# Kernel tuning notes

Hardware: AMD Instinct MI355X
Metric: run time of the kernel (lower is better)

The kernel has to match this reference:

```python
import jax, jax.numpy as jnp
import numpy as np

N_FFT = 1024
HOP = 256
WIN_LENGTH = 1024
B = 16
T = 480000


def setup_inputs() -> dict:
    key = jax.random.key(0)
    k1, k2 = jax.random.split(key)
    x = jax.random.normal(k1, (B, T), dtype=jnp.float32)
    window = jax.random.uniform(k2, (WIN_LENGTH,), dtype=jnp.float32)
    return {"x": x, "window": window}


def _dft_kernels(window):
    # pad window to n_fft if needed (here win_length == n_fft)
    if WIN_LENGTH < N_FFT:
        pl = (N_FFT - WIN_LENGTH) // 2
        window = jnp.pad(window, (pl, N_FFT - WIN_LENGTH - pl))
    n_freq = N_FFT // 2 + 1
    k = jnp.arange(n_freq, dtype=jnp.float32)[:, None]   # [F,1]
    n = jnp.arange(N_FFT, dtype=jnp.float32)[None, :]    # [1,N]
    basis = (2.0 * np.pi / N_FFT) * k * n                # [F,N]
    cos_k = jnp.cos(basis) * window[None, :]
    sin_k = -jnp.sin(basis) * window[None, :]
    return cos_k, sin_k


def reference(x, window):
    pad = N_FFT // 2
    xp = jnp.pad(x, ((0, 0), (pad, pad)), mode="reflect")  # center=True, reflect
    n_frames = (xp.shape[1] - N_FFT) // HOP + 1
    # frame extraction: [n_frames, n_fft] gather indices (strided windows)
    idx = jnp.arange(n_frames)[:, None] * HOP + jnp.arange(N_FFT)[None, :]
    frames = xp[:, idx]                                   # [B, n_frames, n_fft]
    cos_k, sin_k = _dft_kernels(window)                   # [F, n_fft]
    real = jnp.einsum("btn,fn->btf", frames, cos_k)        # [B, n_frames, F]
    imag = jnp.einsum("btn,fn->btf", frames, sin_k)
    return jnp.stack([real, imag], axis=-1)               # [B, n_frames, F, 2]
```

## Files before the change

kernel.cpp:

```cpp
#include <hip/hip_runtime.h>

#define BATCH     16
#define T_LEN     480000
#define PAD       512
#define TPAD      481024
#define HOP       256
#define NFRAMES   1876
#define NOUTROW   1026
#define KTOT      1024
#define NCOLS     1152

#define BM        256
#define BN        128
#define BK        32
#define KSTEPS    (KTOT / BK)
#define MTILES    8
#define ACHUNKS   8288
#define ABYTES    (ACHUNKS * 16)
#define BBUF      8192
#define NBUF      3
#define LDSBYTES  (ABYTES + NBUF * BBUF)
#define XPSTRIDE  493568

typedef __attribute__((ext_vector_type(8))) short short8;
typedef __attribute__((ext_vector_type(4))) float floatx4;

__device__ __forceinline__ unsigned short f2bf(float f) {
  union { float f; unsigned int u; } v; v.f = f;
  unsigned int u = v.u;
  return (unsigned short)((u + 0x7FFFu + ((u >> 16) & 1u)) >> 16);
}

__global__ __launch_bounds__(256) void build_xp(const float* __restrict__ x,
                                                unsigned short* __restrict__ xp) {
  const int i0 = (blockIdx.x * 256 + threadIdx.x) * 8;
  const int b  = blockIdx.y;
  const float* xb = x + (size_t)b * T_LEN;
  const int j0 = i0 - PAD;
  union { short8 v; unsigned short u[8]; } o;
  if (j0 >= 0 && j0 + 8 <= T_LEN) {
    const float4 lo = *(const float4*)(xb + j0);
    const float4 hi = *(const float4*)(xb + j0 + 4);
    o.u[0] = f2bf(lo.x); o.u[1] = f2bf(lo.y); o.u[2] = f2bf(lo.z); o.u[3] = f2bf(lo.w);
    o.u[4] = f2bf(hi.x); o.u[5] = f2bf(hi.y); o.u[6] = f2bf(hi.z); o.u[7] = f2bf(hi.w);
  } else {
#pragma unroll
    for (int e = 0; e < 8; ++e) {
      const int i = i0 + e;
      unsigned short v = 0;
      if (i < TPAD) {
        int j = i - PAD;
        if (j < 0) j = -j;
        if (j >= T_LEN) j = 2 * T_LEN - 2 - j;
        v = f2bf(xb[j]);
      }
      o.u[e] = v;
    }
  }
  *(short8*)(xp + (size_t)b * XPSTRIDE + i0) = o.v;
}

__global__ __launch_bounds__(256) void build_bmat(const float* __restrict__ win,
                                                  unsigned short* __restrict__ bm) {
  const int id = blockIdx.x * 256 + threadIdx.x;
  const int j  = id >> 7;
  const int k0 = (id & 127) * 8;
  union { short8 v; unsigned short u[8]; } o;
  if (j < NOUTROW) {
    const int f = j >> 1;
    const float4 w0 = *(const float4*)(win + k0);
    const float4 w1 = *(const float4*)(win + k0 + 4);
    const float wv[8] = {w0.x, w0.y, w0.z, w0.w, w1.x, w1.y, w1.z, w1.w};
#pragma unroll
    for (int e = 0; e < 8; ++e) {
      const int r = (f * (k0 + e)) & (KTOT - 1);
      const float ang = (float)r * 6.1359231515e-3f;
      const float c = __cosf(ang), s = __sinf(ang);
      o.u[e] = f2bf(((j & 1) ? -s : c) * wv[e]);
    }
  } else {
#pragma unroll
    for (int e = 0; e < 8; ++e) o.u[e] = 0;
  }
  *(short8*)(bm + (size_t)j * KTOT + k0) = o.v;
}

__global__ __launch_bounds__(512, 2) void stft_gemm(const unsigned short* __restrict__ xp,
                                                    const unsigned short* __restrict__ bmat,
                                                    float* __restrict__ out) {
  extern __shared__ unsigned short smem[];
  unsigned short* As = smem;
  unsigned short* Bs = smem + ABYTES / 2;

  const int tid  = threadIdx.x;
  const int lane = tid & 63;
  const int wv   = tid >> 6;
  const int wr   = wv >> 1;
  const int wc   = wv & 1;
  const int L    = lane & 15;
  const int quad = lane >> 4;
  const int b    = blockIdx.x >> 3;
  const int t0   = (blockIdx.x & 7) * BM;
  const int j0   = blockIdx.y * BN;

  const unsigned short* abase = xp + (size_t)b * XPSTRIDE + (size_t)t0 * HOP;

#pragma unroll
  for (int r = 0; r < 17; ++r) {
    const int ci = r * 512 + tid;
    if (ci < ACHUNKS) {
      const int s = ci ^ ((ci >> 5) & 7);
      __builtin_amdgcn_global_load_lds(
          (const __attribute__((address_space(1))) void*)(abase + s * 8),
          (__attribute__((address_space(3))) void*)((char*)As + ci * 16),
          16, 0, 0);
    }
  }

  const int scol = tid & 127, skq = tid >> 7;
  const unsigned short* bsrc = bmat + (size_t)(j0 + scol) * KTOT + skq * 8;
  char* bdst = (char*)Bs + tid * 16;

  __builtin_amdgcn_global_load_lds(
      (const __attribute__((address_space(1))) void*)(bsrc),
      (__attribute__((address_space(3))) void*)(bdst), 16, 0, 0);
  __builtin_amdgcn_global_load_lds(
      (const __attribute__((address_space(1))) void*)(bsrc + BK),
      (__attribute__((address_space(3))) void*)(bdst + BBUF), 16, 0, 0);

  int sbase[4];
  const unsigned short* bfp[4];
#pragma unroll
  for (int t = 0; t < 4; ++t) {
    const int ml = wr * 64 + t * 16 + L;
    sbase[t] = 32 * ml + quad;
    const int n = wc * 64 + t * 16 + L;
    bfp[t] = Bs + ((size_t)quad * 128 + n) * 8;
  }

  floatx4 acc[4][4] = {};

#define GEMM_STEP(KK, CUR, STG, VM)                                            \
  do {                                                                         \
    __builtin_amdgcn_sched_barrier(0);                                         \
    asm volatile("s_waitcnt vmcnt(" #VM ")" ::: "memory");                     \
    __builtin_amdgcn_s_barrier();                                              \
    __builtin_amdgcn_global_load_lds(                                          \
        (const __attribute__((address_space(1))) void*)(bsrc + ((KK) + 2) * BK), \
        (__attribute__((address_space(3))) void*)(bdst + (STG) * BBUF),        \
        16, 0, 0);                                                             \
    const int kc_ = (KK) << 2;                                                 \
    short8 af_[4], bf_[4];                                                     \
    _Pragma("unroll") for (int t = 0; t < 4; ++t) {                            \
      const int s_ = sbase[t] + kc_;                                           \
      const int p_ = s_ ^ ((s_ >> 5) & 7);                                     \
      af_[t] = *(const short8*)&As[p_ * 8];                                    \
      bf_[t] = *(const short8*)(bfp[t] + (CUR) * (BBUF / 2));                  \
    }                                                                          \
    __builtin_amdgcn_s_setprio(1);                                             \
    _Pragma("unroll") for (int ti_ = 0; ti_ < 4; ++ti_)                        \
        _Pragma("unroll") for (int tj_ = 0; tj_ < 4; ++tj_)                    \
            acc[ti_][tj_] = __builtin_amdgcn_mfma_f32_16x16x32_bf16(           \
                af_[ti_], bf_[tj_], acc[ti_][tj_], 0, 0, 0);                   \
    __builtin_amdgcn_s_setprio(0);                                             \
  } while (0)

#define GEMM_TAIL(KK, CUR, VM)                                                 \
  do {                                                                         \
    __builtin_amdgcn_sched_barrier(0);                                         \
    asm volatile("s_waitcnt vmcnt(" #VM ")" ::: "memory");                     \
    __builtin_amdgcn_s_barrier();                                              \
    const int kc_ = (KK) << 2;                                                 \
    short8 af_[4], bf_[4];                                                     \
    _Pragma("unroll") for (int t = 0; t < 4; ++t) {                            \
      const int s_ = sbase[t] + kc_;                                           \
      const int p_ = s_ ^ ((s_ >> 5) & 7);                                     \
      af_[t] = *(const short8*)&As[p_ * 8];                                    \
      bf_[t] = *(const short8*)(bfp[t] + (CUR) * (BBUF / 2));                  \
    }                                                                          \
    __builtin_amdgcn_s_setprio(1);                                             \
    _Pragma("unroll") for (int ti_ = 0; ti_ < 4; ++ti_)                        \
        _Pragma("unroll") for (int tj_ = 0; tj_ < 4; ++tj_)                    \
            acc[ti_][tj_] = __builtin_amdgcn_mfma_f32_16x16x32_bf16(           \
                af_[ti_], bf_[tj_], acc[ti_][tj_], 0, 0, 0);                   \
    __builtin_amdgcn_s_setprio(0);                                             \
  } while (0)

  for (int kk = 0; kk < 10; ++kk) {
    const int k = kk * 3;
    GEMM_STEP(k,     0, 2, 1);
    GEMM_STEP(k + 1, 1, 0, 1);
    GEMM_STEP(k + 2, 2, 1, 1);
  }
  GEMM_TAIL(30, 0, 1);
  GEMM_TAIL(31, 1, 0);

#pragma unroll
  for (int ti = 0; ti < 4; ++ti) {
    const int tb = t0 + wr * 64 + ti * 16 + quad * 4;
#pragma unroll
    for (int tj = 0; tj < 4; ++tj) {
      const int gj = j0 + wc * 64 + tj * 16 + L;
      if (gj < NOUTROW) {
#pragma unroll
        for (int i = 0; i < 4; ++i) {
          const int t = tb + i;
          if (t < NFRAMES)
            out[(size_t)(b * NFRAMES + t) * NOUTROW + gj] = acc[ti][tj][i];
        }
      }
    }
  }
}

extern "C" void kernel_launch(void* const* d_in, const int* in_sizes, int n_in,
                              void* d_out, int out_size, void* d_ws, size_t ws_size,
                              hipStream_t stream) {
  const float* x   = (const float*)d_in[0];
  const float* win = (const float*)d_in[1];
  float* out = (float*)d_out;

  unsigned short* xp   = (unsigned short*)d_ws;
  unsigned short* bmat = xp + (size_t)BATCH * XPSTRIDE;

  (void)hipFuncSetAttribute((const void*)stft_gemm,
                            hipFuncAttributeMaxDynamicSharedMemorySize,
                            LDSBYTES);

  build_xp  <<<dim3(XPSTRIDE / 2048, BATCH), 256, 0, stream>>>(x, xp);
  build_bmat<<<dim3(NCOLS * (KTOT / 8) / 256), 256, 0, stream>>>(win, bmat);
  stft_gemm <<<dim3(BATCH * MTILES, NCOLS / BN), 512, LDSBYTES, stream>>>(xp, bmat, out);
}
```

Before: 241.2 us.

## Switch STFT GEMM to 256x256 tiles with triple-buffered A/B streaming

```diff
diff --git a/kernel.cpp b/kernel.cpp
--- a/kernel.cpp
+++ b/kernel.cpp
@@ -8,22 +8,23 @@
 #define NFRAMES   1876
 #define NOUTROW   1026
 #define KTOT      1024
-#define NCOLS     1152
+#define BCOLS     1152
+#define XPSTRIDE  493568
 
 #define BM        256
-#define BN        128
+#define BN        256
 #define BK        32
-#define KSTEPS    (KTOT / BK)
-#define MTILES    8
-#define ACHUNKS   8288
-#define ABYTES    (ACHUNKS * 16)
-#define BBUF      8192
+#define NTILES    32
+#define TILEA     16384
+#define BUFBYTES  32768
 #define NBUF      3
-#define LDSBYTES  (ABYTES + NBUF * BBUF)
-#define XPSTRIDE  493568
+#define LDSBYTES  (NBUF * BUFBYTES)
 
 typedef __attribute__((ext_vector_type(8))) short short8;
 typedef __attribute__((ext_vector_type(4))) float floatx4;
+
+#define GPTR(p) (const __attribute__((address_space(1))) void*)(p)
+#define LPTR(p) (__attribute__((address_space(3))) void*)(p)
 
 __device__ __forceinline__ unsigned short f2bf(float f) {
   union { float f; unsigned int u; } v; v.f = f;
@@ -88,125 +89,104 @@
 __global__ __launch_bounds__(512, 2) void stft_gemm(const unsigned short* __restrict__ xp,
                                                     const unsigned short* __restrict__ bmat,
                                                     float* __restrict__ out) {
-  extern __shared__ unsigned short smem[];
-  unsigned short* As = smem;
-  unsigned short* Bs = smem + ABYTES / 2;
+  extern __shared__ char smemc[];
 
   const int tid  = threadIdx.x;
   const int lane = tid & 63;
   const int wv   = tid >> 6;
-  const int wr   = wv >> 1;
-  const int wc   = wv & 1;
+  const int wm   = wv >> 2;
+  const int wn   = wv & 3;
   const int L    = lane & 15;
   const int quad = lane >> 4;
   const int b    = blockIdx.x >> 3;
   const int t0   = (blockIdx.x & 7) * BM;
   const int j0   = blockIdx.y * BN;
 
-  const unsigned short* abase = xp + (size_t)b * XPSTRIDE + (size_t)t0 * HOP;
-
-#pragma unroll
-  for (int r = 0; r < 17; ++r) {
-    const int ci = r * 512 + tid;
-    if (ci < ACHUNKS) {
-      const int s = ci ^ ((ci >> 5) & 7);
-      __builtin_amdgcn_global_load_lds(
-          (const __attribute__((address_space(1))) void*)(abase + s * 8),
-          (__attribute__((address_space(3))) void*)((char*)As + ci * 16),
-          16, 0, 0);
-    }
-  }
-
-  const int scol = tid & 127, skq = tid >> 7;
-  const unsigned short* bsrc = bmat + (size_t)(j0 + scol) * KTOT + skq * 8;
-  char* bdst = (char*)Bs + tid * 16;
-
-  __builtin_amdgcn_global_load_lds(
-      (const __attribute__((address_space(1))) void*)(bsrc),
-      (__attribute__((address_space(3))) void*)(bdst), 16, 0, 0);
-  __builtin_amdgcn_global_load_lds(
-      (const __attribute__((address_space(1))) void*)(bsrc + BK),
-      (__attribute__((address_space(3))) void*)(bdst + BBUF), 16, 0, 0);
-
-  int sbase[4];
-  const unsigned short* bfp[4];
-#pragma unroll
-  for (int t = 0; t < 4; ++t) {
-    const int ml = wr * 64 + t * 16 + L;
-    sbase[t] = 32 * ml + quad;
-    const int n = wc * 64 + t * 16 + L;
-    bfp[t] = Bs + ((size_t)quad * 128 + n) * 8;
-  }
-
-  floatx4 acc[4][4] = {};
-
-#define GEMM_STEP(KK, CUR, STG, VM)                                            \
-  do {                                                                         \
-    __builtin_amdgcn_sched_barrier(0);                                         \
+  const int srow = tid & 255;
+  const int skq  = tid >> 8;
+  const unsigned short* asrc =
+      xp + (size_t)b * XPSTRIDE + (size_t)(t0 + srow) * HOP + skq * 8;
+  int jc = j0 + srow;
+  if (jc > BCOLS - 1) jc = BCOLS - 1;
+  const unsigned short* bsrc = bmat + (size_t)jc * KTOT + skq * 8;
+
+#define STAGE_A(KT, S)                                                         \
+  __builtin_amdgcn_global_load_lds(GPTR(asrc + (KT) * BK),                     \
+      LPTR(smemc + (S) * BUFBYTES + tid * 16), 16, 0, 0);                      \
+  __builtin_amdgcn_global_load_lds(GPTR(asrc + (KT) * BK + 16),                \
+      LPTR(smemc + (S) * BUFBYTES + 8192 + tid * 16), 16, 0, 0)
+#define STAGE_B(KT, S)                                                         \
+  __builtin_amdgcn_global_load_lds(GPTR(bsrc + (KT) * BK),                     \
+      LPTR(smemc + (S) * BUFBYTES + TILEA + tid * 16), 16, 0, 0);              \
+  __builtin_amdgcn_global_load_lds(GPTR(bsrc + (KT) * BK + 16),                \
+      LPTR(smemc + (S) * BUFBYTES + TILEA + 8192 + tid * 16), 16, 0, 0)
+
+  const int aoff = (quad * 256 + wm * 128 + L) * 16;
+  const int boff = TILEA + (quad * 256 + wn * 64 + L) * 16;
+
+  floatx4 acc[8][4] = {};
+  short8 af[4], bf[4];
+
+#define PHASE0(C, S, KT2, DOSTAGE)                                             \
+  {                                                                            \
+    const char* tb_ = smemc + (C) * BUFBYTES;                                  \
+    _Pragma("unroll") for (int m = 0; m < 4; ++m)                              \
+      af[m] = *(const short8*)(tb_ + aoff + m * 256);                          \
+    _Pragma("unroll") for (int n = 0; n < 4; ++n)                              \
+      bf[n] = *(const short8*)(tb_ + boff + n * 256);                          \
+    if (DOSTAGE) { STAGE_A(KT2, S); }                                          \
+    __builtin_amdgcn_s_barrier();                                              \
+    __builtin_amdgcn_s_setprio(1);                                             \
+    _Pragma("unroll") for (int m = 0; m < 4; ++m)                              \
+      _Pragma("unroll") for (int n = 0; n < 4; ++n)                            \
+        acc[m][n] = __builtin_amdgcn_mfma_f32_16x16x32_bf16(                   \
+            af[m], bf[n], acc[m][n], 0, 0, 0);                                 \
+    __builtin_amdgcn_s_setprio(0);                                             \
+    __builtin_amdgcn_s_barrier();                                              \
+  }
+#define PHASE1(C, S, KT2, DOSTAGE, VM)                                         \
+  {                                                                            \
+    const char* tb_ = smemc + (C) * BUFBYTES;                                  \
+    _Pragma("unroll") for (int m = 0; m < 4; ++m)                              \
+      af[m] = *(const short8*)(tb_ + aoff + (m + 4) * 256);                    \
+    if (DOSTAGE) { STAGE_B(KT2, S); }                                          \
+    __builtin_amdgcn_s_barrier();                                              \
+    __builtin_amdgcn_s_setprio(1);                                             \
+    _Pragma("unroll") for (int m = 0; m < 4; ++m)                              \
+      _Pragma("unroll") for (int n = 0; n < 4; ++n)                            \
+        acc[m + 4][n] = __builtin_amdgcn_mfma_f32_16x16x32_bf16(               \
+            af[m], bf[n], acc[m + 4][n], 0, 0, 0);                             \
+    __builtin_amdgcn_s_setprio(0);                                             \
     asm volatile("s_waitcnt vmcnt(" #VM ")" ::: "memory");                     \
     __builtin_amdgcn_s_barrier();                                              \
-    __builtin_amdgcn_global_load_lds(                                          \
-        (const __attribute__((address_space(1))) void*)(bsrc + ((KK) + 2) * BK), \
-        (__attribute__((address_space(3))) void*)(bdst + (STG) * BBUF),        \
-        16, 0, 0);                                                             \
-    const int kc_ = (KK) << 2;                                                 \
-    short8 af_[4], bf_[4];                                                     \
-    _Pragma("unroll") for (int t = 0; t < 4; ++t) {                            \
-      const int s_ = sbase[t] + kc_;                                           \
-      const int p_ = s_ ^ ((s_ >> 5) & 7);                                     \
-      af_[t] = *(const short8*)&As[p_ * 8];                                    \
-      bf_[t] = *(const short8*)(bfp[t] + (CUR) * (BBUF / 2));                  \
-    }                                                                          \
-    __builtin_amdgcn_s_setprio(1);                                             \
-    _Pragma("unroll") for (int ti_ = 0; ti_ < 4; ++ti_)                        \
-        _Pragma("unroll") for (int tj_ = 0; tj_ < 4; ++tj_)                    \
-            acc[ti_][tj_] = __builtin_amdgcn_mfma_f32_16x16x32_bf16(           \
-                af_[ti_], bf_[tj_], acc[ti_][tj_], 0, 0, 0);                   \
-    __builtin_amdgcn_s_setprio(0);                                             \
-  } while (0)
-
-#define GEMM_TAIL(KK, CUR, VM)                                                 \
-  do {                                                                         \
-    __builtin_amdgcn_sched_barrier(0);                                         \
-    asm volatile("s_waitcnt vmcnt(" #VM ")" ::: "memory");                     \
-    __builtin_amdgcn_s_barrier();                                              \
-    const int kc_ = (KK) << 2;                                                 \
-    short8 af_[4], bf_[4];                                                     \
-    _Pragma("unroll") for (int t = 0; t < 4; ++t) {                            \
-      const int s_ = sbase[t] + kc_;                                           \
-      const int p_ = s_ ^ ((s_ >> 5) & 7);                                     \
-      af_[t] = *(const short8*)&As[p_ * 8];                                    \
-      bf_[t] = *(const short8*)(bfp[t] + (CUR) * (BBUF / 2));                  \
-    }                                                                          \
-    __builtin_amdgcn_s_setprio(1);                                             \
-    _Pragma("unroll") for (int ti_ = 0; ti_ < 4; ++ti_)                        \
-        _Pragma("unroll") for (int tj_ = 0; tj_ < 4; ++tj_)                    \
-            acc[ti_][tj_] = __builtin_amdgcn_mfma_f32_16x16x32_bf16(           \
-                af_[ti_], bf_[tj_], acc[ti_][tj_], 0, 0, 0);                   \
-    __builtin_amdgcn_s_setprio(0);                                             \
-  } while (0)
-
-  for (int kk = 0; kk < 10; ++kk) {
-    const int k = kk * 3;
-    GEMM_STEP(k,     0, 2, 1);
-    GEMM_STEP(k + 1, 1, 0, 1);
-    GEMM_STEP(k + 2, 2, 1, 1);
-  }
-  GEMM_TAIL(30, 0, 1);
-  GEMM_TAIL(31, 1, 0);
-
-#pragma unroll
-  for (int ti = 0; ti < 4; ++ti) {
-    const int tb = t0 + wr * 64 + ti * 16 + quad * 4;
-#pragma unroll
-    for (int tj = 0; tj < 4; ++tj) {
-      const int gj = j0 + wc * 64 + tj * 16 + L;
+  }
+
+  STAGE_A(0, 0); STAGE_B(0, 0);
+  STAGE_A(1, 1); STAGE_B(1, 1);
+  asm volatile("s_waitcnt vmcnt(4)" ::: "memory");
+  __builtin_amdgcn_s_barrier();
+
+  for (int g = 0; g < 10; ++g) {
+    const int k = 3 * g;
+    PHASE0(0, 2, k + 2, 1);  PHASE1(0, 2, k + 2, 1, 4);
+    PHASE0(1, 0, k + 3, 1);  PHASE1(1, 0, k + 3, 1, 4);
+    PHASE0(2, 1, k + 4, 1);  PHASE1(2, 1, k + 4, 1, 4);
+  }
+  PHASE0(0, 0, 0, 0);  PHASE1(0, 0, 0, 0, 0);
+  PHASE0(1, 0, 0, 0);  PHASE1(1, 0, 0, 0, 0);
+
+#pragma unroll
+  for (int mi = 0; mi < 8; ++mi) {
+    const int tb = t0 + wm * 128 + mi * 16 + quad * 4;
+#pragma unroll
+    for (int ni = 0; ni < 4; ++ni) {
+      const int gj = j0 + wn * 64 + ni * 16 + L;
       if (gj < NOUTROW) {
 #pragma unroll
         for (int i = 0; i < 4; ++i) {
           const int t = tb + i;
           if (t < NFRAMES)
-            out[(size_t)(b * NFRAMES + t) * NOUTROW + gj] = acc[ti][tj][i];
+            out[(size_t)(b * NFRAMES + t) * NOUTROW + gj] = acc[mi][ni][i];
         }
       }
     }
@@ -228,6 +208,6 @@
                             LDSBYTES);
 
   build_xp  <<<dim3(XPSTRIDE / 2048, BATCH), 256, 0, stream>>>(x, xp);
-  build_bmat<<<dim3(NCOLS * (KTOT / 8) / 256), 256, 0, stream>>>(win, bmat);
-  stft_gemm <<<dim3(BATCH * MTILES, NCOLS / BN), 512, LDSBYTES, stream>>>(xp, bmat, out);
-}
+  build_bmat<<<dim3(BCOLS * (KTOT / 8) / 256), 256, 0, stream>>>(win, bmat);
+  stft_gemm <<<dim3(BATCH * 8, 5), 512, LDSBYTES, stream>>>(xp, bmat, out);
+}
```

After: 259.7 us. +7.7%, slower.
